# Kernel tuning notes

Hardware: AMD Instinct MI355X
Metric: run time of the kernel (lower is better)

## Reference

```python
import jax, jax.numpy as jnp
import numpy as np

B, F, P = 16384, 4096, 32
D = F // P
EPS = 1e-5


def setup_inputs() -> dict:
    key = jax.random.key(0)
    ks = jax.random.split(key, 5)
    bound = 1.0 / np.sqrt(D)
    return {
        "x": jax.random.normal(ks[0], (B, F), dtype=jnp.float32),
        "weights1": jax.random.uniform(ks[1], (P, D, D), dtype=jnp.float32, minval=-bound, maxval=bound),
        "bias1": jax.random.uniform(ks[2], (F,), dtype=jnp.float32, minval=-bound, maxval=bound),
        "weights2": jax.random.uniform(ks[3], (P, D, D), dtype=jnp.float32, minval=-bound, maxval=bound),
        "bias2": jax.random.uniform(ks[4], (F,), dtype=jnp.float32, minval=-bound, maxval=bound),
        "gamma1": jnp.ones((F,), dtype=jnp.float32),
        "beta1": jnp.zeros((F,), dtype=jnp.float32),
        "gamma3": jnp.ones((F,), dtype=jnp.float32),
        "beta3": jnp.zeros((F,), dtype=jnp.float32),
    }


def _block_matmul(x, w):
    # x: [B, F] viewed as [B, P, D]; w: [P, D, D] block-diagonal blocks.
    # Equivalent to x @ block_diag(*w) without building the [F, F] matrix.
    xb = x.reshape(x.shape[0], P, D)
    return jnp.einsum("bpd,pde->bpe", xb, w).reshape(x.shape[0], F)


def _batchnorm(y, gamma, beta):
    # Training-mode BatchNorm1d: biased variance over the batch dim.
    mean = jnp.mean(y, axis=0)
    var = jnp.var(y, axis=0)
    return gamma * (y - mean) * jax.lax.rsqrt(var + EPS) + beta


def reference(x, weights1, bias1, weights2, bias2, gamma1, beta1, gamma3, beta3):
    o1 = jnp.tanh(_batchnorm(_block_matmul(x, weights1) + bias1, gamma1, beta1))
    o2 = _block_matmul(o1, weights2) + bias2
    o3 = jnp.tanh(_batchnorm(o2 + x, gamma3, beta3))
    return o3
```

## Files before the change

### kernel.cpp

```cpp
#include <hip/hip_runtime.h>
#include <hip/hip_bf16.h>
#include <cstdint>
#include <cstddef>

#define B_ 16384
#define F_ 4096
#define P_ 32
#define D_ 128
#define STRIPS 32
#define ITERS 8

using f32x4 = __attribute__((ext_vector_type(4))) float;
using s16x8 = __attribute__((ext_vector_type(8))) short;

union abuf { s16x8 v; uint32_t u[4]; };

__device__ inline uint32_t pk_bf16(float a, float b) {
    float2 f; f.x = a; f.y = b;
    union { __hip_bfloat162 h; uint32_t u; } cv;
    cv.h = __float22bfloat162_rn(f);
    return cv.u;
}
__device__ inline float tanh_e(float ze) {
    float e = __builtin_amdgcn_exp2f(ze);
    return 1.f - 2.f * __builtin_amdgcn_rcpf(e + 1.f);
}

__device__ inline void stage_wp(const float* __restrict__ Wp, short* s_w, int tid) {
#pragma unroll
    for (int it = 0; it < 8; ++it) {
        int slot = it * 256 + tid;
        int l15 = slot & 15;
        int l4  = (slot >> 4) & 3;
        int sp  = (slot >> 6) & 3;
        int j   = slot >> 8;
        const float* s0 = Wp + (size_t)(sp * 32 + l4 * 4) * D_ + j * 16 + l15;
        const float* s1 = s0 + (size_t)16 * D_;
        abuf a;
        a.u[0] = pk_bf16(s0[0],            s0[(size_t)D_]);
        a.u[1] = pk_bf16(s0[(size_t)2*D_], s0[(size_t)3*D_]);
        a.u[2] = pk_bf16(s1[0],            s1[(size_t)D_]);
        a.u[3] = pk_bf16(s1[(size_t)2*D_], s1[(size_t)3*D_]);
        *(s16x8*)((char*)s_w + (size_t)slot * 16) = a.v;
    }
}

__global__ __launch_bounds__(256, 3) void k_stats1(
    const float* __restrict__ x, const float* __restrict__ W1,
    float* __restrict__ gsum, float* __restrict__ gsq)
{
    __shared__ short s_w[D_ * D_];
    __shared__ float s_sum[D_], s_sq[D_];
    const int tid = threadIdx.x;
    const int p = blockIdx.x / STRIPS, strip = blockIdx.x % STRIPS;
    stage_wp(W1 + (size_t)p * D_ * D_, s_w, tid);
    if (tid < D_) { s_sum[tid] = 0.f; s_sq[tid] = 0.f; }
    __syncthreads();
    const int wave = tid >> 6, lane = tid & 63;
    const int l15 = lane & 15, l4 = lane >> 4;
    const int ldsb = lane * 16;

    f32x4 csum[8], csq[8];
#pragma unroll
    for (int j = 0; j < 8; ++j) { csum[j] = (f32x4){0,0,0,0}; csq[j] = (f32x4){0,0,0,0}; }

    f32x4 xv[8];
    {
        const float* ap = x + (size_t)((strip * 32 + wave) * 16 + l15) * F_ + p * D_ + l4 * 4;
#pragma unroll
        for (int j = 0; j < 8; ++j) xv[j] = *(const f32x4*)(ap + j * 16);
    }
#pragma unroll
    for (int it = 0; it < ITERS; ++it) {
        abuf a[4];
#pragma unroll
        for (int s = 0; s < 4; ++s) {
            a[s].u[0] = pk_bf16(xv[2*s][0],   xv[2*s][1]);
            a[s].u[1] = pk_bf16(xv[2*s][2],   xv[2*s][3]);
            a[s].u[2] = pk_bf16(xv[2*s+1][0], xv[2*s+1][1]);
            a[s].u[3] = pk_bf16(xv[2*s+1][2], xv[2*s+1][3]);
        }
        if (it + 1 < ITERS) {
            const int g = strip * 32 + (it + 1) * 4 + wave;
            const float* ap = x + (size_t)(g * 16 + l15) * F_ + p * D_ + l4 * 4;
#pragma unroll
            for (int j = 0; j < 8; ++j) xv[j] = *(const f32x4*)(ap + j * 16);
        }
        f32x4 acc[8];
#pragma unroll
        for (int j = 0; j < 8; ++j) acc[j] = (f32x4){0,0,0,0};
#pragma unroll
        for (int s = 0; s < 4; ++s)
#pragma unroll
            for (int j = 0; j < 8; ++j) {
                s16x8 w = *(const s16x8*)((const char*)s_w + (j * 4 + s) * 1024 + ldsb);
                acc[j] = __builtin_amdgcn_mfma_f32_16x16x32_bf16(w, a[s].v, acc[j], 0, 0, 0);
            }
#pragma unroll
        for (int j = 0; j < 8; ++j)
#pragma unroll
            for (int r = 0; r < 4; ++r) {
                float v = acc[j][r];
                csum[j][r] += v;
                csq[j][r] = fmaf(v, v, csq[j][r]);
            }
    }
#pragma unroll
    for (int j = 0; j < 8; ++j)
#pragma unroll
        for (int r = 0; r < 4; ++r) {
            float sm = csum[j][r], q = csq[j][r];
            sm += __shfl_xor(sm, 1); q += __shfl_xor(q, 1);
            sm += __shfl_xor(sm, 2); q += __shfl_xor(q, 2);
            sm += __shfl_xor(sm, 4); q += __shfl_xor(q, 4);
            sm += __shfl_xor(sm, 8); q += __shfl_xor(q, 8);
            if (l15 == 0) {
                atomicAdd(&s_sum[j * 16 + l4 * 4 + r], sm);
                atomicAdd(&s_sq [j * 16 + l4 * 4 + r], q);
            }
        }
    __syncthreads();
    if (tid < D_) {
        atomicAdd(&gsum[p * D_ + tid], s_sum[tid]);
        atomicAdd(&gsq [p * D_ + tid], s_sq[tid]);
    }
}

__global__ __launch_bounds__(256, 2) void k_fused(
    const float* __restrict__ x, float* __restrict__ yf,
    const float* __restrict__ W1, const float* __restrict__ W2,
    const float* __restrict__ sce, const float* __restrict__ she,
    float* __restrict__ gsum, float* __restrict__ gsq)
{
    __shared__ short s_w1[D_ * D_];
    __shared__ short s_w2[D_ * D_];
    __shared__ float s_sc[D_], s_sh[D_];
    __shared__ float s_sum[D_], s_sq[D_];
    const int tid = threadIdx.x;
    const int p = blockIdx.x / STRIPS, strip = blockIdx.x % STRIPS;
    stage_wp(W1 + (size_t)p * D_ * D_, s_w1, tid);
    stage_wp(W2 + (size_t)p * D_ * D_, s_w2, tid);
    if (tid < D_) {
        s_sc[tid] = sce[p * D_ + tid];
        s_sh[tid] = she[p * D_ + tid];
        s_sum[tid] = 0.f; s_sq[tid] = 0.f;
    }
    __syncthreads();
    const int wave = tid >> 6, lane = tid & 63;
    const int l15 = lane & 15, l4 = lane >> 4;
    const int ldsb = lane * 16;

    f32x4 csum[8], csq[8];
#pragma unroll
    for (int j = 0; j < 8; ++j) { csum[j] = (f32x4){0,0,0,0}; csq[j] = (f32x4){0,0,0,0}; }

    auto LOADX = [&](f32x4 (&xv)[8], int it) {
        const int g = strip * 32 + it * 4 + wave;
        const float* ap = x + (size_t)(g * 16 + l15) * F_ + p * D_ + l4 * 4;
#pragma unroll
        for (int j = 0; j < 8; ++j)
            xv[j] = *(const f32x4*)(ap + j * 16);
    };

    auto TILE = [&](f32x4 (&xv)[8], int it) {
        abuf a[4];
#pragma unroll
        for (int s = 0; s < 4; ++s) {
            a[s].u[0] = pk_bf16(xv[2*s][0],   xv[2*s][1]);
            a[s].u[1] = pk_bf16(xv[2*s][2],   xv[2*s][3]);
            a[s].u[2] = pk_bf16(xv[2*s+1][0], xv[2*s+1][1]);
            a[s].u[3] = pk_bf16(xv[2*s+1][2], xv[2*s+1][3]);
        }
        f32x4 acc[8];
#pragma unroll
        for (int j = 0; j < 8; ++j) acc[j] = (f32x4){0,0,0,0};
#pragma unroll
        for (int s = 0; s < 4; ++s)
#pragma unroll
            for (int j = 0; j < 8; ++j) {
                s16x8 w = *(const s16x8*)((const char*)s_w1 + (j * 4 + s) * 1024 + ldsb);
                acc[j] = __builtin_amdgcn_mfma_f32_16x16x32_bf16(w, a[s].v, acc[j], 0, 0, 0);
            }
#pragma unroll
        for (int sp = 0; sp < 4; ++sp) {
            const int kb = sp * 32 + l4 * 4;
            f32x4 sc0 = *(const f32x4*)&s_sc[kb], sc1 = *(const f32x4*)&s_sc[kb + 16];
            f32x4 sh0 = *(const f32x4*)&s_sh[kb], sh1 = *(const f32x4*)&s_sh[kb + 16];
            float t0[4], t1[4];
#pragma unroll
            for (int q = 0; q < 4; ++q) {
                t0[q] = tanh_e(fmaf(acc[2*sp][q],   sc0[q], sh0[q]));
                t1[q] = tanh_e(fmaf(acc[2*sp+1][q], sc1[q], sh1[q]));
            }
            a[sp].u[0] = pk_bf16(t0[0], t0[1]);
            a[sp].u[1] = pk_bf16(t0[2], t0[3]);
            a[sp].u[2] = pk_bf16(t1[0], t1[1]);
            a[sp].u[3] = pk_bf16(t1[2], t1[3]);
        }
#pragma unroll
        for (int j = 0; j < 8; ++j) acc[j] = (f32x4){0,0,0,0};
#pragma unroll
        for (int sp = 0; sp < 4; ++sp)
#pragma unroll
            for (int j = 0; j < 8; ++j) {
                s16x8 w = *(const s16x8*)((const char*)s_w2 + (j * 4 + sp) * 1024 + ldsb);
                acc[j] = __builtin_amdgcn_mfma_f32_16x16x32_bf16(w, a[sp].v, acc[j], 0, 0, 0);
            }
        const int g = strip * 32 + it * 4 + wave;
        float* rp = yf + (size_t)(g * 16 + l15) * F_ + p * D_ + l4 * 4;
#pragma unroll
        for (int j = 0; j < 8; ++j) {
            f32x4 o;
#pragma unroll
            for (int r = 0; r < 4; ++r) {
                float v = acc[j][r] + xv[j][r];
                o[r] = v;
                csum[j][r] += v;
                csq[j][r] = fmaf(v, v, csq[j][r]);
            }
            __builtin_nontemporal_store(o, (f32x4*)(rp + j * 16));
        }
    };

    f32x4 xv0[8], xv1[8];
    LOADX(xv0, 0);
#pragma unroll
    for (int h = 0; h < 4; ++h) {
        LOADX(xv1, 2 * h + 1);
        TILE(xv0, 2 * h);
        if (h < 3) LOADX(xv0, 2 * h + 2);
        TILE(xv1, 2 * h + 1);
    }

#pragma unroll
    for (int j = 0; j < 8; ++j)
#pragma unroll
        for (int r = 0; r < 4; ++r) {
            float sm = csum[j][r], q = csq[j][r];
            sm += __shfl_xor(sm, 1); q += __shfl_xor(q, 1);
            sm += __shfl_xor(sm, 2); q += __shfl_xor(q, 2);
            sm += __shfl_xor(sm, 4); q += __shfl_xor(q, 4);
            sm += __shfl_xor(sm, 8); q += __shfl_xor(q, 8);
            if (l15 == 0) {
                atomicAdd(&s_sum[j * 16 + l4 * 4 + r], sm);
                atomicAdd(&s_sq [j * 16 + l4 * 4 + r], q);
            }
        }
    __syncthreads();
    if (tid < D_) {
        atomicAdd(&gsum[p * D_ + tid], s_sum[tid]);
        atomicAdd(&gsq [p * D_ + tid], s_sq[tid]);
    }
}

__global__ void k_finalize(const float* __restrict__ sum,
                           const float* __restrict__ sumsq,
                           const float* __restrict__ gamma,
                           const float* __restrict__ beta,
                           float* __restrict__ sce, float* __restrict__ she)
{
    const float L2E2 = 2.f * 1.44269504088896340736f;
    int f = blockIdx.x * blockDim.x + threadIdx.x;
    if (f < F_) {
        float mean = sum[f] * (1.f / B_);
        float var  = sumsq[f] * (1.f / B_) - mean * mean;
        float rstd = rsqrtf(var + 1e-5f);
        float sc = gamma[f] * rstd;
        sce[f] = L2E2 * sc;
        she[f] = L2E2 * (beta[f] - mean * sc);
    }
}

__global__ void k_bn_tanh(float* yb, const float* __restrict__ sce,
                          const float* __restrict__ she)
{
    const size_t n4 = (size_t)B_ * F_ / 4;
    size_t i = (size_t)blockIdx.x * blockDim.x + threadIdx.x;
    const size_t stride = (size_t)gridDim.x * blockDim.x;
    for (; i < n4; i += stride) {
        f32x4 v = ((const f32x4*)yb)[i];
        int col = (int)((i * 4) & (F_ - 1));
        f32x4 sc = *(const f32x4*)(sce + col);
        f32x4 sh = *(const f32x4*)(she + col);
        f32x4 r;
#pragma unroll
        for (int t = 0; t < 4; ++t) r[t] = tanh_e(fmaf(v[t], sc[t], sh[t]));
        __builtin_nontemporal_store(r, (f32x4*)yb + i);
    }
}

extern "C" void kernel_launch(void* const* d_in, const int* in_sizes, int n_in,
                              void* d_out, int out_size, void* d_ws, size_t ws_size,
                              hipStream_t stream) {
    const float* x      = (const float*)d_in[0];
    const float* W1     = (const float*)d_in[1];
    const float* W2     = (const float*)d_in[3];
    const float* gamma1 = (const float*)d_in[5];
    const float* beta1  = (const float*)d_in[6];
    const float* gamma3 = (const float*)d_in[7];
    const float* beta3  = (const float*)d_in[8];

    float* yf = (float*)d_out;
    float* S  = (float*)d_ws;
    float* sum1 = S;
    float* sq1  = S + 4096;
    float* sum3 = S + 8192;
    float* sq3  = S + 12288;
    float* sce1 = S + 16384;
    float* she1 = S + 20480;
    float* sce3 = S + 24576;
    float* she3 = S + 28672;

    hipMemsetAsync(d_ws, 0, 4 * 4096 * sizeof(float), stream);

    k_stats1<<<P_ * STRIPS, 256, 0, stream>>>(x, W1, sum1, sq1);
    k_finalize<<<F_ / 256, 256, 0, stream>>>(sum1, sq1, gamma1, beta1, sce1, she1);
    k_fused<<<P_ * STRIPS, 256, 0, stream>>>(x, yf, W1, W2, sce1, she1, sum3, sq3);
    k_finalize<<<F_ / 256, 256, 0, stream>>>(sum3, sq3, gamma3, beta3, sce3, she3);
    k_bn_tanh<<<4096, 256, 0, stream>>>(yf, sce3, she3);
}
```

Before: 624.8 us.

## Recompute both block matmuls in a final pass instead of storing and re-reading the intermediate

The fused kernel no longer writes the pre-BN residual sum to global memory. A stats-only pass accumulates BN3 statistics, then a second pass recomputes both block matmuls and applies BN3 plus tanh directly to the output. This replaces a full write plus a read-modify-write of the 256MB intermediate with an extra read of x and extra MFMA work. Blocks also grow to 512 threads (8 waves), with 16 strips per partition, and k_stats1 gains double-buffered x loads.

```diff
diff --git a/kernel.cpp b/kernel.cpp
--- a/kernel.cpp
+++ b/kernel.cpp
@@ -7,7 +7,8 @@
 #define F_ 4096
 #define P_ 32
 #define D_ 128
-#define STRIPS 32
+#define BLOCKS 512
+#define WPB 8
 #define ITERS 8
 
 using f32x4 = __attribute__((ext_vector_type(4))) float;
@@ -28,8 +29,8 @@
 
 __device__ inline void stage_wp(const float* __restrict__ Wp, short* s_w, int tid) {
 #pragma unroll
-    for (int it = 0; it < 8; ++it) {
-        int slot = it * 256 + tid;
+    for (int it = 0; it < 4; ++it) {
+        int slot = it * 512 + tid;
         int l15 = slot & 15;
         int l4  = (slot >> 4) & 3;
         int sp  = (slot >> 6) & 3;
@@ -45,14 +46,14 @@
     }
 }
 
-__global__ __launch_bounds__(256, 3) void k_stats1(
+__global__ __launch_bounds__(512, 4) void k_stats1(
     const float* __restrict__ x, const float* __restrict__ W1,
     float* __restrict__ gsum, float* __restrict__ gsq)
 {
     __shared__ short s_w[D_ * D_];
     __shared__ float s_sum[D_], s_sq[D_];
     const int tid = threadIdx.x;
-    const int p = blockIdx.x / STRIPS, strip = blockIdx.x % STRIPS;
+    const int p = blockIdx.x >> 4, strip = blockIdx.x & 15;
     stage_wp(W1 + (size_t)p * D_ * D_, s_w, tid);
     if (tid < D_) { s_sum[tid] = 0.f; s_sq[tid] = 0.f; }
     __syncthreads();
@@ -64,14 +65,15 @@
 #pragma unroll
     for (int j = 0; j < 8; ++j) { csum[j] = (f32x4){0,0,0,0}; csq[j] = (f32x4){0,0,0,0}; }
 
-    f32x4 xv[8];
-    {
-        const float* ap = x + (size_t)((strip * 32 + wave) * 16 + l15) * F_ + p * D_ + l4 * 4;
-#pragma unroll
-        for (int j = 0; j < 8; ++j) xv[j] = *(const f32x4*)(ap + j * 16);
-    }
-#pragma unroll
-    for (int it = 0; it < ITERS; ++it) {
+    auto LOADX = [&](f32x4 (&xv)[8], int it) {
+        const int g = strip * 64 + it * 8 + wave;
+        const float* ap = x + (size_t)(g * 16 + l15) * F_ + p * D_ + l4 * 4;
+#pragma unroll
+        for (int j = 0; j < 8; ++j)
+            xv[j] = *(const f32x4*)(ap + j * 16);
+    };
+
+    auto TILE = [&](f32x4 (&xv)[8]) {
         abuf a[4];
 #pragma unroll
         for (int s = 0; s < 4; ++s) {
@@ -80,12 +82,6 @@
             a[s].u[2] = pk_bf16(xv[2*s+1][0], xv[2*s+1][1]);
             a[s].u[3] = pk_bf16(xv[2*s+1][2], xv[2*s+1][3]);
         }
-        if (it + 1 < ITERS) {
-            const int g = strip * 32 + (it + 1) * 4 + wave;
-            const float* ap = x + (size_t)(g * 16 + l15) * F_ + p * D_ + l4 * 4;
-#pragma unroll
-            for (int j = 0; j < 8; ++j) xv[j] = *(const f32x4*)(ap + j * 16);
-        }
         f32x4 acc[8];
 #pragma unroll
         for (int j = 0; j < 8; ++j) acc[j] = (f32x4){0,0,0,0};
@@ -104,7 +100,18 @@
                 csum[j][r] += v;
                 csq[j][r] = fmaf(v, v, csq[j][r]);
             }
-    }
+    };
+
+    f32x4 xv0[8], xv1[8];
+    LOADX(xv0, 0);
+#pragma unroll
+    for (int h = 0; h < 4; ++h) {
+        LOADX(xv1, 2 * h + 1);
+        TILE(xv0);
+        if (h < 3) LOADX(xv0, 2 * h + 2);
+        TILE(xv1);
+    }
+
 #pragma unroll
     for (int j = 0; j < 8; ++j)
 #pragma unroll
@@ -126,24 +133,31 @@
     }
 }
 
-__global__ __launch_bounds__(256, 2) void k_fused(
-    const float* __restrict__ x, float* __restrict__ yf,
+template<bool OUT>
+__global__ __launch_bounds__(512, 4) void k_pass(
+    const float* __restrict__ x, float* __restrict__ out,
     const float* __restrict__ W1, const float* __restrict__ W2,
-    const float* __restrict__ sce, const float* __restrict__ she,
+    const float* __restrict__ sce1, const float* __restrict__ she1,
+    const float* __restrict__ sce3, const float* __restrict__ she3,
     float* __restrict__ gsum, float* __restrict__ gsq)
 {
     __shared__ short s_w1[D_ * D_];
     __shared__ short s_w2[D_ * D_];
-    __shared__ float s_sc[D_], s_sh[D_];
-    __shared__ float s_sum[D_], s_sq[D_];
+    __shared__ float s_sc1[D_], s_sh1[D_];
+    __shared__ float s_a[D_], s_b[D_];
     const int tid = threadIdx.x;
-    const int p = blockIdx.x / STRIPS, strip = blockIdx.x % STRIPS;
+    const int p = blockIdx.x >> 4, strip = blockIdx.x & 15;
     stage_wp(W1 + (size_t)p * D_ * D_, s_w1, tid);
     stage_wp(W2 + (size_t)p * D_ * D_, s_w2, tid);
     if (tid < D_) {
-        s_sc[tid] = sce[p * D_ + tid];
-        s_sh[tid] = she[p * D_ + tid];
-        s_sum[tid] = 0.f; s_sq[tid] = 0.f;
+        s_sc1[tid] = sce1[p * D_ + tid];
+        s_sh1[tid] = she1[p * D_ + tid];
+        if (OUT) {
+            s_a[tid] = sce3[p * D_ + tid];
+            s_b[tid] = she3[p * D_ + tid];
+        } else {
+            s_a[tid] = 0.f; s_b[tid] = 0.f;
+        }
     }
     __syncthreads();
     const int wave = tid >> 6, lane = tid & 63;
@@ -151,11 +165,13 @@
     const int ldsb = lane * 16;
 
     f32x4 csum[8], csq[8];
-#pragma unroll
-    for (int j = 0; j < 8; ++j) { csum[j] = (f32x4){0,0,0,0}; csq[j] = (f32x4){0,0,0,0}; }
+    if (!OUT) {
+#pragma unroll
+        for (int j = 0; j < 8; ++j) { csum[j] = (f32x4){0,0,0,0}; csq[j] = (f32x4){0,0,0,0}; }
+    }
 
     auto LOADX = [&](f32x4 (&xv)[8], int it) {
-        const int g = strip * 32 + it * 4 + wave;
+        const int g = strip * 64 + it * 8 + wave;
         const float* ap = x + (size_t)(g * 16 + l15) * F_ + p * D_ + l4 * 4;
 #pragma unroll
         for (int j = 0; j < 8; ++j)
@@ -184,8 +200,8 @@
 #pragma unroll
         for (int sp = 0; sp < 4; ++sp) {
             const int kb = sp * 32 + l4 * 4;
-            f32x4 sc0 = *(const f32x4*)&s_sc[kb], sc1 = *(const f32x4*)&s_sc[kb + 16];
-            f32x4 sh0 = *(const f32x4*)&s_sh[kb], sh1 = *(const f32x4*)&s_sh[kb + 16];
+            f32x4 sc0 = *(const f32x4*)&s_sc1[kb], sc1 = *(const f32x4*)&s_sc1[kb + 16];
+            f32x4 sh0 = *(const f32x4*)&s_sh1[kb], sh1 = *(const f32x4*)&s_sh1[kb + 16];
             float t0[4], t1[4];
 #pragma unroll
             for (int q = 0; q < 4; ++q) {
@@ -206,19 +222,28 @@
                 s16x8 w = *(const s16x8*)((const char*)s_w2 + (j * 4 + sp) * 1024 + ldsb);
                 acc[j] = __builtin_amdgcn_mfma_f32_16x16x32_bf16(w, a[sp].v, acc[j], 0, 0, 0);
             }
-        const int g = strip * 32 + it * 4 + wave;
-        float* rp = yf + (size_t)(g * 16 + l15) * F_ + p * D_ + l4 * 4;
-#pragma unroll
-        for (int j = 0; j < 8; ++j) {
-            f32x4 o;
-#pragma unroll
-            for (int r = 0; r < 4; ++r) {
-                float v = acc[j][r] + xv[j][r];
-                o[r] = v;
-                csum[j][r] += v;
-                csq[j][r] = fmaf(v, v, csq[j][r]);
-            }
-            __builtin_nontemporal_store(o, (f32x4*)(rp + j * 16));
+        if (OUT) {
+            const int g = strip * 64 + it * 8 + wave;
+            float* rp = out + (size_t)(g * 16 + l15) * F_ + p * D_ + l4 * 4;
+#pragma unroll
+            for (int j = 0; j < 8; ++j) {
+                f32x4 sc3 = *(const f32x4*)&s_a[j * 16 + l4 * 4];
+                f32x4 sh3 = *(const f32x4*)&s_b[j * 16 + l4 * 4];
+                f32x4 o;
+#pragma unroll
+                for (int r = 0; r < 4; ++r)
+                    o[r] = tanh_e(fmaf(acc[j][r] + xv[j][r], sc3[r], sh3[r]));
+                __builtin_nontemporal_store(o, (f32x4*)(rp + j * 16));
+            }
+        } else {
+#pragma unroll
+            for (int j = 0; j < 8; ++j)
+#pragma unroll
+                for (int r = 0; r < 4; ++r) {
+                    float v = acc[j][r] + xv[j][r];
+                    csum[j][r] += v;
+                    csq[j][r] = fmaf(v, v, csq[j][r]);
+                }
         }
     };
 
@@ -232,24 +257,26 @@
         TILE(xv1, 2 * h + 1);
     }
 
-#pragma unroll
-    for (int j = 0; j < 8; ++j)
-#pragma unroll
-        for (int r = 0; r < 4; ++r) {
-            float sm = csum[j][r], q = csq[j][r];
-            sm += __shfl_xor(sm, 1); q += __shfl_xor(q, 1);
-            sm += __shfl_xor(sm, 2); q += __shfl_xor(q, 2);
-            sm += __shfl_xor(sm, 4); q += __shfl_xor(q, 4);
-            sm += __shfl_xor(sm, 8); q += __shfl_xor(q, 8);
-            if (l15 == 0) {
-                atomicAdd(&s_sum[j * 16 + l4 * 4 + r], sm);
-                atomicAdd(&s_sq [j * 16 + l4 * 4 + r], q);
-            }
-        }
-    __syncthreads();
-    if (tid < D_) {
-        atomicAdd(&gsum[p * D_ + tid], s_sum[tid]);
-        atomicAdd(&gsq [p * D_ + tid], s_sq[tid]);
+    if (!OUT) {
+#pragma unroll
+        for (int j = 0; j < 8; ++j)
+#pragma unroll
+            for (int r = 0; r < 4; ++r) {
+                float sm = csum[j][r], q = csq[j][r];
+                sm += __shfl_xor(sm, 1); q += __shfl_xor(q, 1);
+                sm += __shfl_xor(sm, 2); q += __shfl_xor(q, 2);
+                sm += __shfl_xor(sm, 4); q += __shfl_xor(q, 4);
+                sm += __shfl_xor(sm, 8); q += __shfl_xor(q, 8);
+                if (l15 == 0) {
+                    atomicAdd(&s_a[j * 16 + l4 * 4 + r], sm);
+                    atomicAdd(&s_b[j * 16 + l4 * 4 + r], q);
+                }
+            }
+        __syncthreads();
+        if (tid < D_) {
+            atomicAdd(&gsum[p * D_ + tid], s_a[tid]);
+            atomicAdd(&gsq [p * D_ + tid], s_b[tid]);
+        }
     }
 }
 
@@ -271,24 +298,6 @@
     }
 }
 
-__global__ void k_bn_tanh(float* yb, const float* __restrict__ sce,
-                          const float* __restrict__ she)
-{
-    const size_t n4 = (size_t)B_ * F_ / 4;
-    size_t i = (size_t)blockIdx.x * blockDim.x + threadIdx.x;
-    const size_t stride = (size_t)gridDim.x * blockDim.x;
-    for (; i < n4; i += stride) {
-        f32x4 v = ((const f32x4*)yb)[i];
-        int col = (int)((i * 4) & (F_ - 1));
-        f32x4 sc = *(const f32x4*)(sce + col);
-        f32x4 sh = *(const f32x4*)(she + col);
-        f32x4 r;
-#pragma unroll
-        for (int t = 0; t < 4; ++t) r[t] = tanh_e(fmaf(v[t], sc[t], sh[t]));
-        __builtin_nontemporal_store(r, (f32x4*)yb + i);
-    }
-}
-
 extern "C" void kernel_launch(void* const* d_in, const int* in_sizes, int n_in,
                               void* d_out, int out_size, void* d_ws, size_t ws_size,
                               hipStream_t stream) {
@@ -300,7 +309,7 @@
     const float* gamma3 = (const float*)d_in[7];
     const float* beta3  = (const float*)d_in[8];
 
-    float* yf = (float*)d_out;
+    float* out = (float*)d_out;
     float* S  = (float*)d_ws;
     float* sum1 = S;
     float* sq1  = S + 4096;
@@ -313,9 +322,9 @@
 
     hipMemsetAsync(d_ws, 0, 4 * 4096 * sizeof(float), stream);
 
-    k_stats1<<<P_ * STRIPS, 256, 0, stream>>>(x, W1, sum1, sq1);
+    k_stats1<<<BLOCKS, 512, 0, stream>>>(x, W1, sum1, sq1);
     k_finalize<<<F_ / 256, 256, 0, stream>>>(sum1, sq1, gamma1, beta1, sce1, she1);
-    k_fused<<<P_ * STRIPS, 256, 0, stream>>>(x, yf, W1, W2, sce1, she1, sum3, sq3);
+    k_pass<false><<<BLOCKS, 512, 0, stream>>>(x, out, W1, W2, sce1, she1, sce3, she3, sum3, sq3);
     k_finalize<<<F_ / 256, 256, 0, stream>>>(sum3, sq3, gamma3, beta3, sce3, she3);
-    k_bn_tanh<<<4096, 256, 0, stream>>>(yf, sce3, she3);
-}
+    k_pass<true><<<BLOCKS, 512, 0, stream>>>(x, out, W1, W2, sce1, she1, sce3, she3, sum3, sq3);
+}
```

After: 1.468 ms. 135% more time.
